# Kernel tuning notes

Hardware: AMD Instinct MI355X
Metric: run time of the kernel (lower is better)

## Reference

```python
import jax, jax.numpy as jnp
import numpy as np

IN_DIM = 300   # GloVe embedding dim
MEM = 150      # TreeLSTM memory dim
K = 4          # children per internal node (complete K-ary tree)
D = 9          # number of levels (leaves = level 0, root = level D-1)
SIZES = [K ** (D - 1 - d) for d in range(D)]  # nodes per level, leaves first
N = sum(SIZES)  # 87381 total nodes


def setup_inputs() -> dict:
    key = jax.random.key(0)
    ks = jax.random.split(key, 18)
    s_in = 1.0 / np.sqrt(IN_DIM)
    s_m = 1.0 / np.sqrt(MEM)
    inp = {"embs": jax.random.normal(ks[0], (N, IN_DIM), jnp.float32)}
    i = 1
    for nm in ["ix", "fx", "ux", "ox"]:  # input->mem linears
        inp["W_" + nm] = jax.random.uniform(ks[i], (IN_DIM, MEM), jnp.float32, -s_in, s_in); i += 1
        inp["b_" + nm] = jax.random.uniform(ks[i], (MEM,), jnp.float32, -s_in, s_in); i += 1
    for nm in ["ih", "fh", "uh", "oh"]:  # mem->mem linears
        inp["W_" + nm] = jax.random.uniform(ks[i], (MEM, MEM), jnp.float32, -s_m, s_m); i += 1
        inp["b_" + nm] = jax.random.uniform(ks[i], (MEM,), jnp.float32, -s_m, s_m); i += 1
    return inp


def reference(embs, W_ix, b_ix, W_fx, b_fx, W_ux, b_ux, W_ox, b_ox,
              W_ih, b_ih, W_fh, b_fh, W_uh, b_uh, W_oh, b_oh):
    """Level-batched Child-Sum TreeLSTM over a complete K-ary forest.
    Nodes are stored leaves-first; children of parent p at level d are
    nodes p*K .. p*K+K-1 of level d-1. Returns h for all N nodes (root last)."""
    off = 0
    h_prev = c_prev = None
    h_all = []
    for d in range(D):
        n = SIZES[d]
        x = embs[off:off + n]                       # (n, IN_DIM)
        if d == 0:
            # leaves: zero child state -> child_h_sum = 0, f*child_c = 0
            h_sum = jnp.zeros((n, MEM), embs.dtype)
            fc = jnp.zeros((n, MEM), embs.dtype)
        else:
            ch = h_prev.reshape(n, K, MEM)          # child h, (n, K, MEM)
            cc = c_prev.reshape(n, K, MEM)          # child c
            h_sum = ch.sum(axis=1)                  # child-sum of h
            # per-child forget gate: fh(child_h) + fx(x)
            f = jax.nn.sigmoid(jnp.einsum('nkm,mp->nkp', ch, W_fh) + b_fh
                               + (x @ W_fx + b_fx)[:, None, :])
            fc = (f * cc).sum(axis=1)
        i_g = jax.nn.sigmoid(x @ W_ix + b_ix + h_sum @ W_ih + b_ih)
        o_g = jax.nn.sigmoid(x @ W_ox + b_ox + h_sum @ W_oh + b_oh)
        u = jnp.tanh(x @ W_ux + b_ux + h_sum @ W_uh + b_uh)
        c = i_g * u + fc
        h = o_g * jnp.tanh(c)
        h_all.append(h)
        h_prev, c_prev = h, c
        off += n
    return jnp.concatenate(h_all, axis=0)           # (N, MEM)
```

## Files before the change

kernel.cpp:

```cpp
#include <hip/hip_runtime.h>

#define IN_DIM 300
#define MEM    150
#define GP     160
#define GW     640
#define KX     300
#define KXP    320
#define KH     160
#define NLEAF  65536
#define NTOT   87381
#define DEPTH  9

static const int SIZES[DEPTH] = {65536,16384,4096,1024,256,64,16,4,1};
static const int OFF[DEPTH]   = {0,65536,81920,86016,87040,87296,87360,87376,87380};

typedef __attribute__((ext_vector_type(8))) short short8;
typedef __attribute__((ext_vector_type(4))) float f32x4;

__device__ __forceinline__ float sigf(float x) { return 1.0f / (1.0f + __expf(-x)); }
__device__ __forceinline__ float tanhf_fast(float x) {
    float e = __expf(2.0f * x);
    return 1.0f - 2.0f / (e + 1.0f);
}
__device__ __forceinline__ unsigned short f2bf(float f) {
    union { float f; unsigned u; } v; v.f = f;
    unsigned r = v.u + 0x7FFF + ((v.u >> 16) & 1);
    return (unsigned short)(r >> 16);
}
__device__ __forceinline__ float bf2f(unsigned short u) {
    union { unsigned u; float f; } v; v.u = ((unsigned)u) << 16; return v.f;
}

typedef const __attribute__((address_space(1))) unsigned int* as1_u32p;
typedef __attribute__((address_space(3))) unsigned int* as3_u32p;
__device__ __forceinline__ void gl_lds16(const unsigned short* g, unsigned short* l) {
    __builtin_amdgcn_global_load_lds((as1_u32p)g, (as3_u32p)l, 16, 0, 0);
}

__global__ void pack_weights(const float* __restrict__ Wix, const float* __restrict__ Wfx,
                             const float* __restrict__ Wux, const float* __restrict__ Wox,
                             const float* __restrict__ bix, const float* __restrict__ bfx,
                             const float* __restrict__ bux, const float* __restrict__ box,
                             const float* __restrict__ Wih, const float* __restrict__ Wfh,
                             const float* __restrict__ Wuh, const float* __restrict__ Woh,
                             const float* __restrict__ bfh,
                             unsigned short* __restrict__ W4xT, unsigned short* __restrict__ W4hT,
                             float* __restrict__ b4x, float* __restrict__ b4hf)
{
    int stride = gridDim.x * blockDim.x;
    int tid = blockIdx.x * blockDim.x + threadIdx.x;
    for (int idx = tid; idx < GW * KXP; idx += stride) {
        int c = idx / KXP, k = idx - c * KXP;
        int g = c / GP, j = c - g * GP;
        const float* W = (g == 0) ? Wix : (g == 1) ? Wfx : (g == 2) ? Wux : Wox;
        W4xT[idx] = (j < MEM && k < KX) ? f2bf(W[k * MEM + j]) : (unsigned short)0;
    }
    for (int idx = tid; idx < GW * KH; idx += stride) {
        int c = idx / KH, k = idx - c * KH;
        int g = c / GP, j = c - g * GP;
        const float* W = (g == 0) ? Wih : (g == 1) ? Wfh : (g == 2) ? Wuh : Woh;
        W4hT[idx] = (j < MEM && k < MEM) ? f2bf(W[k * MEM + j]) : (unsigned short)0;
    }
    for (int idx = tid; idx < GW; idx += stride) {
        int g = idx / GP, j = idx - g * GP;
        const float* b = (g == 0) ? bix : (g == 1) ? bfx : (g == 2) ? bux : box;
        b4x[idx]  = (j < MEM) ? b[j] : 0.0f;
        b4hf[idx] = (g == 1 && j < MEM) ? bfh[j] : 0.0f;
    }
}

__global__ void conv_embs(const float* __restrict__ embs, unsigned short* __restrict__ Abf)
{
    int idx = blockIdx.x * 256 + threadIdx.x;
    if (idx >= NTOT * (KXP / 8)) return;
    int n = idx / (KXP / 8), c = idx - n * (KXP / 8);
    int c0 = c * 8;
    unsigned short v[8];
    if (c0 + 8 <= KX) {
        const float4* p = (const float4*)(embs + (size_t)n * KX + c0);
        float4 f0 = p[0], f1 = p[1];
        v[0]=f2bf(f0.x); v[1]=f2bf(f0.y); v[2]=f2bf(f0.z); v[3]=f2bf(f0.w);
        v[4]=f2bf(f1.x); v[5]=f2bf(f1.y); v[6]=f2bf(f1.z); v[7]=f2bf(f1.w);
    } else {
        const float* row = embs + (size_t)n * KX;
        #pragma unroll
        for (int j = 0; j < 8; ++j) {
            int col = c0 + j;
            v[j] = (col < KX) ? f2bf(row[col]) : (unsigned short)0;
        }
    }
    *(short8*)&Abf[(size_t)n * KXP + c0] = *(short8*)v;
}

template<int KPAD>
__global__ __launch_bounds__(256) void gemm_lds(
    const unsigned short* __restrict__ A, int M,
    const unsigned short* __restrict__ BT,
    const float* __restrict__ bias,
    unsigned short* __restrict__ Cout)
{
    __shared__ __align__(16) unsigned short As[2][128 * 32];
    __shared__ __align__(16) unsigned short Bs[2][128 * 32];

    const int nwg = gridDim.x;
    const int orig = blockIdx.x;
    const int qq = nwg >> 3, rr = nwg & 7;
    const int xcd = orig & 7, lin = orig >> 3;
    const int dd = (xcd < rr ? xcd * (qq + 1) : rr * (qq + 1) + (xcd - rr) * qq) + lin;
    const int mtile = dd / 5, ntile = dd - mtile * 5;

    const int t = threadIdx.x;
    const int m0 = mtile * 128, n0 = ntile * 128;
    const int l = t & 63, w = t >> 6;
    const int l15 = l & 15, q = l >> 4;
    const int wm = (w & 1) * 64, wn = (w >> 1) * 64;

    const int srow = t >> 2;
    const int scol = ((t & 3) ^ (srow & 3)) * 8;
    int gr0 = m0 + srow;      if (gr0 >= M) gr0 = M - 1;
    int gr1 = m0 + 64 + srow; if (gr1 >= M) gr1 = M - 1;
    const unsigned short* a0 = A + (size_t)gr0 * KPAD + scol;
    const unsigned short* a1 = A + (size_t)gr1 * KPAD + scol;
    const unsigned short* b0 = BT + (size_t)(n0 + srow) * KPAD + scol;
    const unsigned short* b1 = BT + (size_t)(n0 + 64 + srow) * KPAD + scol;

    f32x4 acc[4][4];
    #pragma unroll
    for (int i = 0; i < 4; ++i)
        #pragma unroll
        for (int j = 0; j < 4; ++j)
            acc[i][j] = (f32x4){0.f, 0.f, 0.f, 0.f};

    const int kiters = KPAD >> 5;
    gl_lds16(a0, &As[0][t * 8]);
    gl_lds16(a1, &As[0][2048 + t * 8]);
    gl_lds16(b0, &Bs[0][t * 8]);
    gl_lds16(b1, &Bs[0][2048 + t * 8]);
    __syncthreads();

    int cur = 0;
    for (int kt = 0; kt < kiters; ++kt) {
        if (kt + 1 < kiters) {
            const int ko = (kt + 1) << 5;
            const int nb = cur ^ 1;
            gl_lds16(a0 + ko, &As[nb][t * 8]);
            gl_lds16(a1 + ko, &As[nb][2048 + t * 8]);
            gl_lds16(b0 + ko, &Bs[nb][t * 8]);
            gl_lds16(b1 + ko, &Bs[nb][2048 + t * 8]);
        }
        short8 a[4], b[4];
        const int csw = (q ^ (l15 & 3)) * 8;
        #pragma unroll
        for (int i = 0; i < 4; ++i)
            a[i] = *(const short8*)&As[cur][(wm + i * 16 + l15) * 32 + csw];
        #pragma unroll
        for (int j = 0; j < 4; ++j)
            b[j] = *(const short8*)&Bs[cur][(wn + j * 16 + l15) * 32 + csw];
        #pragma unroll
        for (int i = 0; i < 4; ++i)
            #pragma unroll
            for (int j = 0; j < 4; ++j)
                acc[i][j] = __builtin_amdgcn_mfma_f32_16x16x32_bf16(a[i], b[j], acc[i][j], 0, 0, 0);
        __syncthreads();
        cur ^= 1;
    }

    float bj[4];
    #pragma unroll
    for (int j = 0; j < 4; ++j) bj[j] = bias[n0 + wn + j * 16 + l15];
    #pragma unroll
    for (int i = 0; i < 4; ++i) {
        #pragma unroll
        for (int r = 0; r < 4; ++r) {
            int grow = m0 + wm + i * 16 + q * 4 + r;
            if (grow < M) {
                unsigned short* crow = Cout + (size_t)grow * GW;
                #pragma unroll
                for (int j = 0; j < 4; ++j)
                    crow[n0 + wn + j * 16 + l15] = f2bf(acc[i][j][r] + bj[j]);
            }
        }
    }
}

__global__ void leaf_ew(const unsigned short* __restrict__ PG,
                        const float* __restrict__ bih, const float* __restrict__ buh,
                        const float* __restrict__ boh,
                        float* __restrict__ out, float* __restrict__ C,
                        unsigned short* __restrict__ Hbf)
{
    int idx = blockIdx.x * 256 + threadIdx.x;
    if (idx >= NLEAF * MEM) return;
    int n = idx / MEM, m = idx - n * MEM;
    const unsigned short* row = PG + (size_t)n * GW;
    float ip = bf2f(row[m])          + bih[m];
    float up = bf2f(row[2 * GP + m]) + buh[m];
    float op = bf2f(row[3 * GP + m]) + boh[m];
    float i = sigf(ip), u = tanhf_fast(up), o = sigf(op);
    float c = i * u;
    float h = o * tanhf_fast(c);
    out[idx] = h;
    C[idx] = c;
    Hbf[(size_t)n * KH + m] = f2bf(h);
    if (m < KH - MEM) Hbf[(size_t)n * KH + MEM + m] = 0;
}

__global__ void level_ew(const unsigned short* __restrict__ G,
                         const unsigned short* __restrict__ P,
                         const float* __restrict__ Cprev,
                         const float* __restrict__ bih, const float* __restrict__ buh,
                         const float* __restrict__ boh,
                         float* __restrict__ outRow, float* __restrict__ Crow,
                         unsigned short* __restrict__ HbfRow, int n)
{
    int idx = blockIdx.x * 256 + threadIdx.x;
    if (idx >= n * MEM) return;
    int nn = idx / MEM, m = idx - nn * MEM;
    const unsigned short* xr = P + (size_t)nn * GW;
    float ip = bf2f(xr[m]) + bih[m];
    float fx = bf2f(xr[GP + m]);
    float up = bf2f(xr[2 * GP + m]) + buh[m];
    float op = bf2f(xr[3 * GP + m]) + boh[m];
    float fc = 0.0f;
    #pragma unroll
    for (int k = 0; k < 4; ++k) {
        const unsigned short* gr = G + (size_t)(4 * nn + k) * GW;
        ip += bf2f(gr[m]);
        up += bf2f(gr[2 * GP + m]);
        op += bf2f(gr[3 * GP + m]);
        float f = sigf(fx + bf2f(gr[GP + m]));
        fc += f * Cprev[(4 * nn + k) * MEM + m];
    }
    float i = sigf(ip), u = tanhf_fast(up), o = sigf(op);
    float c = i * u + fc;
    float h = o * tanhf_fast(c);
    outRow[idx] = h;
    Crow[idx] = c;
    HbfRow[(size_t)nn * KH + m] = f2bf(h);
    if (m < KH - MEM) HbfRow[(size_t)nn * KH + MEM + m] = 0;
}

extern "C" void kernel_launch(void* const* d_in, const int* in_sizes, int n_in,
                              void* d_out, int out_size, void* d_ws, size_t ws_size,
                              hipStream_t stream)
{
    (void)in_sizes; (void)n_in; (void)out_size;
    const float* embs = (const float*)d_in[0];
    const float* Wix = (const float*)d_in[1];  const float* bix = (const float*)d_in[2];
    const float* Wfx = (const float*)d_in[3];  const float* bfx = (const float*)d_in[4];
    const float* Wux = (const float*)d_in[5];  const float* bux = (const float*)d_in[6];
    const float* Wox = (const float*)d_in[7];  const float* box = (const float*)d_in[8];
    const float* Wih = (const float*)d_in[9];  const float* bih = (const float*)d_in[10];
    const float* Wfh = (const float*)d_in[11]; const float* bfh = (const float*)d_in[12];
    const float* Wuh = (const float*)d_in[13]; const float* buh = (const float*)d_in[14];
    const float* Woh = (const float*)d_in[15]; const float* boh = (const float*)d_in[16];
    float* out = (float*)d_out;

    char* p = (char*)d_ws;
    auto alloc = [&](size_t bytes) -> char* {
        char* r = p;
        p += (bytes + 255) & ~(size_t)255;
        return r;
    };
    unsigned short* PG   = (unsigned short*)alloc((size_t)NTOT * GW * 2);
    float*          C    = (float*)alloc((size_t)NTOT * MEM * 4);
    unsigned short* Hbf  = (unsigned short*)alloc((size_t)NTOT * KH * 2);
    unsigned short* W4xT = (unsigned short*)alloc((size_t)GW * KXP * 2);
    unsigned short* W4hT = (unsigned short*)alloc((size_t)GW * KH * 2);
    float*          b4x  = (float*)alloc(GW * 4);
    float*          b4hf = (float*)alloc(GW * 4);
    if ((size_t)(p - (char*)d_ws) > ws_size) return;

    unsigned short* Abf = (unsigned short*)C;

    pack_weights<<<128, 256, 0, stream>>>(Wix, Wfx, Wux, Wox, bix, bfx, bux, box,
                                          Wih, Wfh, Wuh, Woh, bfh,
                                          W4xT, W4hT, b4x, b4hf);

    conv_embs<<<(NTOT * (KXP / 8) + 255) / 256, 256, 0, stream>>>(embs, Abf);

    {
        int mt = (NTOT + 127) / 128;
        gemm_lds<KXP><<<mt * 5, 256, 0, stream>>>(Abf, NTOT, W4xT, b4x, PG);
    }

    leaf_ew<<<(NLEAF * MEM + 255) / 256, 256, 0, stream>>>(PG, bih, buh, boh, out, C, Hbf);

    for (int d = 1; d < DEPTH; ++d) {
        int nprev = SIZES[d - 1];
        int n = SIZES[d];
        int mt = (nprev + 127) / 128;
        gemm_lds<KH><<<mt * 5, 256, 0, stream>>>(
            Hbf + (size_t)OFF[d - 1] * KH, nprev, W4hT, b4hf, PG);
        level_ew<<<(n * MEM + 255) / 256, 256, 0, stream>>>(
            PG, PG + (size_t)OFF[d] * GW,
            C + (size_t)OFF[d - 1] * MEM,
            bih, buh, boh,
            out + (size_t)OFF[d] * MEM, C + (size_t)OFF[d] * MEM,
            Hbf + (size_t)OFF[d] * KH, n);
    }
}
```

Baseline: 431.1 us.

## Deepen GEMM LDS pipeline to four stages with explicit vmcnt waits

Replaces the double-buffered direct-to-LDS load loop in the bf16 MFMA GEMM with a 4-buffer ring that keeps three K-slices of global loads in flight. It uses hand-placed s_waitcnt vmcnt thresholds and raw s_barrier instead of __syncthreads, and fully unrolls the K loop. It also raises wave priority around the MFMA block. The aim is to hide global-load latency better in the input-projection GEMM. In exchange LDS use doubles to 64KB, which may reduce occupancy, and correctness depends on exact vmcnt counting.

After: 440.7 us. 2.2% more time.

```diff
diff --git a/kernel.cpp b/kernel.cpp
--- a/kernel.cpp
+++ b/kernel.cpp
@@ -99,8 +99,8 @@
     const float* __restrict__ bias,
     unsigned short* __restrict__ Cout)
 {
-    __shared__ __align__(16) unsigned short As[2][128 * 32];
-    __shared__ __align__(16) unsigned short Bs[2][128 * 32];
+    __shared__ __align__(16) unsigned short As[4][4096];
+    __shared__ __align__(16) unsigned short Bs[4][4096];
 
     const int nwg = gridDim.x;
     const int orig = blockIdx.x;
@@ -131,38 +131,49 @@
         for (int j = 0; j < 4; ++j)
             acc[i][j] = (f32x4){0.f, 0.f, 0.f, 0.f};
 
-    const int kiters = KPAD >> 5;
-    gl_lds16(a0, &As[0][t * 8]);
-    gl_lds16(a1, &As[0][2048 + t * 8]);
-    gl_lds16(b0, &Bs[0][t * 8]);
-    gl_lds16(b1, &Bs[0][2048 + t * 8]);
-    __syncthreads();
-
-    int cur = 0;
-    for (int kt = 0; kt < kiters; ++kt) {
-        if (kt + 1 < kiters) {
-            const int ko = (kt + 1) << 5;
-            const int nb = cur ^ 1;
-            gl_lds16(a0 + ko, &As[nb][t * 8]);
-            gl_lds16(a1 + ko, &As[nb][2048 + t * 8]);
-            gl_lds16(b0 + ko, &Bs[nb][t * 8]);
-            gl_lds16(b1 + ko, &Bs[nb][2048 + t * 8]);
-        }
+    auto issue = [&](int s) {
+        const int ko = s << 5;
+        const int b = s & 3;
+        gl_lds16(a0 + ko, &As[b][t * 8]);
+        gl_lds16(a1 + ko, &As[b][2048 + t * 8]);
+        gl_lds16(b0 + ko, &Bs[b][t * 8]);
+        gl_lds16(b1 + ko, &Bs[b][2048 + t * 8]);
+    };
+
+    const int NST = KPAD >> 5;
+    issue(0); issue(1); issue(2);
+
+    #pragma unroll
+    for (int kt = 0; kt < NST; ++kt) {
+        if (kt + 3 < NST) issue(kt + 3);
+        __builtin_amdgcn_sched_barrier(0);
+        const int rem = NST - 1 - kt;
+        if (rem >= 3)      asm volatile("s_waitcnt vmcnt(12)" ::: "memory");
+        else if (rem == 2) asm volatile("s_waitcnt vmcnt(8)" ::: "memory");
+        else if (rem == 1) asm volatile("s_waitcnt vmcnt(4)" ::: "memory");
+        else               asm volatile("s_waitcnt vmcnt(0)" ::: "memory");
+        __builtin_amdgcn_s_barrier();
+        __builtin_amdgcn_sched_barrier(0);
+
+        const unsigned short* Ab = As[kt & 3];
+        const unsigned short* Bb = Bs[kt & 3];
         short8 a[4], b[4];
         const int csw = (q ^ (l15 & 3)) * 8;
         #pragma unroll
         for (int i = 0; i < 4; ++i)
-            a[i] = *(const short8*)&As[cur][(wm + i * 16 + l15) * 32 + csw];
+            a[i] = *(const short8*)&Ab[(wm + i * 16 + l15) * 32 + csw];
         #pragma unroll
         for (int j = 0; j < 4; ++j)
-            b[j] = *(const short8*)&Bs[cur][(wn + j * 16 + l15) * 32 + csw];
+            b[j] = *(const short8*)&Bb[(wn + j * 16 + l15) * 32 + csw];
+        __builtin_amdgcn_s_setprio(1);
         #pragma unroll
         for (int i = 0; i < 4; ++i)
             #pragma unroll
             for (int j = 0; j < 4; ++j)
                 acc[i][j] = __builtin_amdgcn_mfma_f32_16x16x32_bf16(a[i], b[j], acc[i][j], 0, 0, 0);
-        __syncthreads();
-        cur ^= 1;
+        __builtin_amdgcn_s_setprio(0);
+        __builtin_amdgcn_sched_barrier(0);
+        __builtin_amdgcn_s_barrier();
     }
 
     float bj[4];
```

## Fuse gate elementwise into GEMM epilogues via interleaved gate layout

Applied to the files above, without the earlier changes.

Reorders the packed weight columns so the four gates of each hidden unit sit next to each other. Each 128-column GEMM tile then holds every gate for 32 hidden units, so the leaf and level elementwise TreeLSTM math can run in the GEMM epilogue from LDS, removing the separate leaf_ew and level_ew kernels and the round trip of the per-child gate matrix through global memory. Leaf rows of the input projection are never written to PG, and the bf16 embedding buffer now reuses PG instead of C. The trade-off is a heavier epilogue with extra LDS staging and a barrier, and the aliasing of Abf onto PG must stay safe while tiles overwrite rows that other blocks may still be reading.

After: 371.8 us. 1.16x faster.

```diff
diff --git a/kernel.cpp b/kernel.cpp
--- a/kernel.cpp
+++ b/kernel.cpp
@@ -1,8 +1,6 @@
 #include <hip/hip_runtime.h>
 
-#define IN_DIM 300
 #define MEM    150
-#define GP     160
 #define GW     640
 #define KX     300
 #define KXP    320
@@ -51,18 +49,18 @@
     int tid = blockIdx.x * blockDim.x + threadIdx.x;
     for (int idx = tid; idx < GW * KXP; idx += stride) {
         int c = idx / KXP, k = idx - c * KXP;
-        int g = c / GP, j = c - g * GP;
+        int j = c >> 2, g = c & 3;
         const float* W = (g == 0) ? Wix : (g == 1) ? Wfx : (g == 2) ? Wux : Wox;
         W4xT[idx] = (j < MEM && k < KX) ? f2bf(W[k * MEM + j]) : (unsigned short)0;
     }
     for (int idx = tid; idx < GW * KH; idx += stride) {
         int c = idx / KH, k = idx - c * KH;
-        int g = c / GP, j = c - g * GP;
+        int j = c >> 2, g = c & 3;
         const float* W = (g == 0) ? Wih : (g == 1) ? Wfh : (g == 2) ? Wuh : Woh;
         W4hT[idx] = (j < MEM && k < MEM) ? f2bf(W[k * MEM + j]) : (unsigned short)0;
     }
     for (int idx = tid; idx < GW; idx += stride) {
-        int g = idx / GP, j = idx - g * GP;
+        int j = idx >> 2, g = idx & 3;
         const float* b = (g == 0) ? bix : (g == 1) ? bfx : (g == 2) ? bux : box;
         b4x[idx]  = (j < MEM) ? b[j] : 0.0f;
         b4hf[idx] = (g == 1 && j < MEM) ? bfh[j] : 0.0f;
@@ -92,15 +90,19 @@
     *(short8*)&Abf[(size_t)n * KXP + c0] = *(short8*)v;
 }
 
-template<int KPAD>
-__global__ __launch_bounds__(256) void gemm_lds(
-    const unsigned short* __restrict__ A, int M,
+__global__ __launch_bounds__(256) void gemm_xproj(
+    const unsigned short* __restrict__ A,
     const unsigned short* __restrict__ BT,
     const float* __restrict__ bias,
-    unsigned short* __restrict__ Cout)
+    unsigned short* __restrict__ PG,
+    const float* __restrict__ bih, const float* __restrict__ buh,
+    const float* __restrict__ boh,
+    float* __restrict__ outLeaf, float* __restrict__ CLeaf,
+    unsigned short* __restrict__ HbfLeaf)
 {
-    __shared__ __align__(16) unsigned short As[2][128 * 32];
-    __shared__ __align__(16) unsigned short Bs[2][128 * 32];
+    __shared__ __align__(16) unsigned short lds[16384];
+    unsigned short* As = lds;
+    unsigned short* Bs = lds + 8192;
 
     const int nwg = gridDim.x;
     const int orig = blockIdx.x;
@@ -117,12 +119,12 @@
 
     const int srow = t >> 2;
     const int scol = ((t & 3) ^ (srow & 3)) * 8;
-    int gr0 = m0 + srow;      if (gr0 >= M) gr0 = M - 1;
-    int gr1 = m0 + 64 + srow; if (gr1 >= M) gr1 = M - 1;
-    const unsigned short* a0 = A + (size_t)gr0 * KPAD + scol;
-    const unsigned short* a1 = A + (size_t)gr1 * KPAD + scol;
-    const unsigned short* b0 = BT + (size_t)(n0 + srow) * KPAD + scol;
-    const unsigned short* b1 = BT + (size_t)(n0 + 64 + srow) * KPAD + scol;
+    int gr0 = m0 + srow;      if (gr0 >= NTOT) gr0 = NTOT - 1;
+    int gr1 = m0 + 64 + srow; if (gr1 >= NTOT) gr1 = NTOT - 1;
+    const unsigned short* a0 = A + (size_t)gr0 * KXP + scol;
+    const unsigned short* a1 = A + (size_t)gr1 * KXP + scol;
+    const unsigned short* b0 = BT + (size_t)(n0 + srow) * KXP + scol;
+    const unsigned short* b1 = BT + (size_t)(n0 + 64 + srow) * KXP + scol;
 
     f32x4 acc[4][4];
     #pragma unroll
@@ -131,31 +133,31 @@
         for (int j = 0; j < 4; ++j)
             acc[i][j] = (f32x4){0.f, 0.f, 0.f, 0.f};
 
-    const int kiters = KPAD >> 5;
-    gl_lds16(a0, &As[0][t * 8]);
-    gl_lds16(a1, &As[0][2048 + t * 8]);
-    gl_lds16(b0, &Bs[0][t * 8]);
-    gl_lds16(b1, &Bs[0][2048 + t * 8]);
+    gl_lds16(a0, As + t * 8);
+    gl_lds16(a1, As + 2048 + t * 8);
+    gl_lds16(b0, Bs + t * 8);
+    gl_lds16(b1, Bs + 2048 + t * 8);
     __syncthreads();
 
     int cur = 0;
+    const int kiters = KXP >> 5;
     for (int kt = 0; kt < kiters; ++kt) {
         if (kt + 1 < kiters) {
             const int ko = (kt + 1) << 5;
             const int nb = cur ^ 1;
-            gl_lds16(a0 + ko, &As[nb][t * 8]);
-            gl_lds16(a1 + ko, &As[nb][2048 + t * 8]);
-            gl_lds16(b0 + ko, &Bs[nb][t * 8]);
-            gl_lds16(b1 + ko, &Bs[nb][2048 + t * 8]);
+            gl_lds16(a0 + ko, As + nb * 4096 + t * 8);
+            gl_lds16(a1 + ko, As + nb * 4096 + 2048 + t * 8);
+            gl_lds16(b0 + ko, Bs + nb * 4096 + t * 8);
+            gl_lds16(b1 + ko, Bs + nb * 4096 + 2048 + t * 8);
         }
         short8 a[4], b[4];
         const int csw = (q ^ (l15 & 3)) * 8;
         #pragma unroll
         for (int i = 0; i < 4; ++i)
-            a[i] = *(const short8*)&As[cur][(wm + i * 16 + l15) * 32 + csw];
-        #pragma unroll
-        for (int j = 0; j < 4; ++j)
-            b[j] = *(const short8*)&Bs[cur][(wn + j * 16 + l15) * 32 + csw];
+            a[i] = *(const short8*)&As[cur * 4096 + (wm + i * 16 + l15) * 32 + csw];
+        #pragma unroll
+        for (int j = 0; j < 4; ++j)
+            b[j] = *(const short8*)&Bs[cur * 4096 + (wn + j * 16 + l15) * 32 + csw];
         #pragma unroll
         for (int i = 0; i < 4; ++i)
             #pragma unroll
@@ -169,75 +171,174 @@
     #pragma unroll
     for (int j = 0; j < 4; ++j) bj[j] = bias[n0 + wn + j * 16 + l15];
     #pragma unroll
-    for (int i = 0; i < 4; ++i) {
-        #pragma unroll
-        for (int r = 0; r < 4; ++r) {
-            int grow = m0 + wm + i * 16 + q * 4 + r;
-            if (grow < M) {
-                unsigned short* crow = Cout + (size_t)grow * GW;
-                #pragma unroll
-                for (int j = 0; j < 4; ++j)
-                    crow[n0 + wn + j * 16 + l15] = f2bf(acc[i][j][r] + bj[j]);
+    for (int i = 0; i < 4; ++i)
+        #pragma unroll
+        for (int j = 0; j < 4; ++j)
+            #pragma unroll
+            for (int r = 0; r < 4; ++r)
+                lds[(wm + i * 16 + q * 4 + r) * 128 + wn + j * 16 + l15] =
+                    f2bf(acc[i][j][r] + bj[j]);
+    __syncthreads();
+
+    if (m0 < NLEAF) {
+        #pragma unroll
+        for (int s = 0; s < 16; ++s) {
+            int idx = (s << 8) + t;
+            int row = idx >> 5, jl = idx & 31;
+            int grow = m0 + row;
+            int j = ntile * 32 + jl;
+            const unsigned short* g4 = &lds[row * 128 + jl * 4];
+            if (j < MEM) {
+                float gi = bf2f(g4[0]) + bih[j];
+                float gu = bf2f(g4[2]) + buh[j];
+                float go = bf2f(g4[3]) + boh[j];
+                float iv = sigf(gi), uv = tanhf_fast(gu), ov = sigf(go);
+                float c = iv * uv;
+                float h = ov * tanhf_fast(c);
+                outLeaf[(size_t)grow * MEM + j] = h;
+                CLeaf[(size_t)grow * MEM + j] = c;
+                HbfLeaf[(size_t)grow * KH + j] = f2bf(h);
+            } else if (j < KH) {
+                HbfLeaf[(size_t)grow * KH + j] = 0;
             }
         }
-    }
-}
-
-__global__ void leaf_ew(const unsigned short* __restrict__ PG,
-                        const float* __restrict__ bih, const float* __restrict__ buh,
-                        const float* __restrict__ boh,
-                        float* __restrict__ out, float* __restrict__ C,
-                        unsigned short* __restrict__ Hbf)
+    } else {
+        int row = t >> 1, half = t & 1;
+        int grow = m0 + row;
+        if (grow < NTOT) {
+            const unsigned short* src = &lds[row * 128 + half * 64];
+            unsigned short* dst = PG + (size_t)grow * GW + n0 + half * 64;
+            #pragma unroll
+            for (int c8 = 0; c8 < 8; ++c8)
+                *(short8*)(dst + c8 * 8) = *(const short8*)(src + c8 * 8);
+        }
+    }
+}
+
+__global__ __launch_bounds__(256) void gemm_level(
+    const unsigned short* __restrict__ Hprev, int nprev, int npar,
+    const unsigned short* __restrict__ BT, const float* __restrict__ bias,
+    const unsigned short* __restrict__ P,
+    const float* __restrict__ Cprev,
+    const float* __restrict__ bih, const float* __restrict__ buh,
+    const float* __restrict__ boh,
+    float* __restrict__ outRow, float* __restrict__ Crow,
+    unsigned short* __restrict__ HbfRow)
 {
-    int idx = blockIdx.x * 256 + threadIdx.x;
-    if (idx >= NLEAF * MEM) return;
-    int n = idx / MEM, m = idx - n * MEM;
-    const unsigned short* row = PG + (size_t)n * GW;
-    float ip = bf2f(row[m])          + bih[m];
-    float up = bf2f(row[2 * GP + m]) + buh[m];
-    float op = bf2f(row[3 * GP + m]) + boh[m];
-    float i = sigf(ip), u = tanhf_fast(up), o = sigf(op);
-    float c = i * u;
-    float h = o * tanhf_fast(c);
-    out[idx] = h;
-    C[idx] = c;
-    Hbf[(size_t)n * KH + m] = f2bf(h);
-    if (m < KH - MEM) Hbf[(size_t)n * KH + MEM + m] = 0;
-}
-
-__global__ void level_ew(const unsigned short* __restrict__ G,
-                         const unsigned short* __restrict__ P,
-                         const float* __restrict__ Cprev,
-                         const float* __restrict__ bih, const float* __restrict__ buh,
-                         const float* __restrict__ boh,
-                         float* __restrict__ outRow, float* __restrict__ Crow,
-                         unsigned short* __restrict__ HbfRow, int n)
-{
-    int idx = blockIdx.x * 256 + threadIdx.x;
-    if (idx >= n * MEM) return;
-    int nn = idx / MEM, m = idx - nn * MEM;
-    const unsigned short* xr = P + (size_t)nn * GW;
-    float ip = bf2f(xr[m]) + bih[m];
-    float fx = bf2f(xr[GP + m]);
-    float up = bf2f(xr[2 * GP + m]) + buh[m];
-    float op = bf2f(xr[3 * GP + m]) + boh[m];
-    float fc = 0.0f;
-    #pragma unroll
-    for (int k = 0; k < 4; ++k) {
-        const unsigned short* gr = G + (size_t)(4 * nn + k) * GW;
-        ip += bf2f(gr[m]);
-        up += bf2f(gr[2 * GP + m]);
-        op += bf2f(gr[3 * GP + m]);
-        float f = sigf(fx + bf2f(gr[GP + m]));
-        fc += f * Cprev[(4 * nn + k) * MEM + m];
-    }
-    float i = sigf(ip), u = tanhf_fast(up), o = sigf(op);
-    float c = i * u + fc;
-    float h = o * tanhf_fast(c);
-    outRow[idx] = h;
-    Crow[idx] = c;
-    HbfRow[(size_t)nn * KH + m] = f2bf(h);
-    if (m < KH - MEM) HbfRow[(size_t)nn * KH + MEM + m] = 0;
+    __shared__ __align__(16) unsigned short lds[16384];
+    unsigned short* As = lds;
+    unsigned short* Bs = lds + 8192;
+
+    const int nwg = gridDim.x;
+    const int orig = blockIdx.x;
+    const int qq = nwg >> 3, rr = nwg & 7;
+    const int xcd = orig & 7, lin = orig >> 3;
+    const int dd = (xcd < rr ? xcd * (qq + 1) : rr * (qq + 1) + (xcd - rr) * qq) + lin;
+    const int mtile = dd / 5, ntile = dd - mtile * 5;
+
+    const int t = threadIdx.x;
+    const int m0 = mtile * 128, n0 = ntile * 128;
+    const int l = t & 63, w = t >> 6;
+    const int l15 = l & 15, q = l >> 4;
+    const int wm = (w & 1) * 64, wn = (w >> 1) * 64;
+
+    const int srow = t >> 2;
+    const int scol = ((t & 3) ^ (srow & 3)) * 8;
+    int gr0 = m0 + srow;      if (gr0 >= nprev) gr0 = nprev - 1;
+    int gr1 = m0 + 64 + srow; if (gr1 >= nprev) gr1 = nprev - 1;
+    const unsigned short* a0 = Hprev + (size_t)gr0 * KH + scol;
+    const unsigned short* a1 = Hprev + (size_t)gr1 * KH + scol;
+    const unsigned short* b0 = BT + (size_t)(n0 + srow) * KH + scol;
+    const unsigned short* b1 = BT + (size_t)(n0 + 64 + srow) * KH + scol;
+
+    f32x4 acc[4][4];
+    #pragma unroll
+    for (int i = 0; i < 4; ++i)
+        #pragma unroll
+        for (int j = 0; j < 4; ++j)
+            acc[i][j] = (f32x4){0.f, 0.f, 0.f, 0.f};
+
+    gl_lds16(a0, As + t * 8);
+    gl_lds16(a1, As + 2048 + t * 8);
+    gl_lds16(b0, Bs + t * 8);
+    gl_lds16(b1, Bs + 2048 + t * 8);
+    __syncthreads();
+
+    int cur = 0;
+    const int kiters = KH >> 5;
+    for (int kt = 0; kt < kiters; ++kt) {
+        if (kt + 1 < kiters) {
+            const int ko = (kt + 1) << 5;
+            const int nb = cur ^ 1;
+            gl_lds16(a0 + ko, As + nb * 4096 + t * 8);
+            gl_lds16(a1 + ko, As + nb * 4096 + 2048 + t * 8);
+            gl_lds16(b0 + ko, Bs + nb * 4096 + t * 8);
+            gl_lds16(b1 + ko, Bs + nb * 4096 + 2048 + t * 8);
+        }
+        short8 a[4], b[4];
+        const int csw = (q ^ (l15 & 3)) * 8;
+        #pragma unroll
+        for (int i = 0; i < 4; ++i)
+            a[i] = *(const short8*)&As[cur * 4096 + (wm + i * 16 + l15) * 32 + csw];
+        #pragma unroll
+        for (int j = 0; j < 4; ++j)
+            b[j] = *(const short8*)&Bs[cur * 4096 + (wn + j * 16 + l15) * 32 + csw];
+        #pragma unroll
+        for (int i = 0; i < 4; ++i)
+            #pragma unroll
+            for (int j = 0; j < 4; ++j)
+                acc[i][j] = __builtin_amdgcn_mfma_f32_16x16x32_bf16(a[i], b[j], acc[i][j], 0, 0, 0);
+        __syncthreads();
+        cur ^= 1;
+    }
+
+    float bj[4];
+    #pragma unroll
+    for (int j = 0; j < 4; ++j) bj[j] = bias[n0 + wn + j * 16 + l15];
+    #pragma unroll
+    for (int i = 0; i < 4; ++i)
+        #pragma unroll
+        for (int j = 0; j < 4; ++j)
+            #pragma unroll
+            for (int r = 0; r < 4; ++r)
+                lds[(wm + i * 16 + q * 4 + r) * 128 + wn + j * 16 + l15] =
+                    f2bf(acc[i][j][r] + bj[j]);
+    __syncthreads();
+
+    const int pp0 = m0 >> 2;
+    #pragma unroll
+    for (int s = 0; s < 4; ++s) {
+        int idx = (s << 8) + t;
+        int pl = idx >> 5, jl = idx & 31;
+        int par = pp0 + pl;
+        if (par >= npar) continue;
+        int j = ntile * 32 + jl;
+        if (j < MEM) {
+            const unsigned short* xr = P + (size_t)par * GW + 4 * j;
+            float ip = bf2f(xr[0]) + bih[j];
+            float fx = bf2f(xr[1]);
+            float up = bf2f(xr[2]) + buh[j];
+            float op = bf2f(xr[3]) + boh[j];
+            float fc = 0.0f;
+            #pragma unroll
+            for (int k = 0; k < 4; ++k) {
+                const unsigned short* g4 = &lds[(pl * 4 + k) * 128 + jl * 4];
+                ip += bf2f(g4[0]);
+                up += bf2f(g4[2]);
+                op += bf2f(g4[3]);
+                float f = sigf(fx + bf2f(g4[1]));
+                fc += f * Cprev[(size_t)(4 * par + k) * MEM + j];
+            }
+            float iv = sigf(ip), uv = tanhf_fast(up), ov = sigf(op);
+            float c = iv * uv + fc;
+            float h = ov * tanhf_fast(c);
+            outRow[(size_t)par * MEM + j] = h;
+            Crow[(size_t)par * MEM + j] = c;
+            HbfRow[(size_t)par * KH + j] = f2bf(h);
+        } else if (j < KH) {
+            HbfRow[(size_t)par * KH + j] = 0;
+        }
+    }
 }
 
 extern "C" void kernel_launch(void* const* d_in, const int* in_sizes, int n_in,
@@ -271,7 +372,7 @@
     float*          b4hf = (float*)alloc(GW * 4);
     if ((size_t)(p - (char*)d_ws) > ws_size) return;
 
-    unsigned short* Abf = (unsigned short*)C;
+    unsigned short* Abf = PG;
 
     pack_weights<<<128, 256, 0, stream>>>(Wix, Wfx, Wux, Wox, bix, bfx, bux, box,
                                           Wih, Wfh, Wuh, Woh, bfh,
@@ -281,22 +382,21 @@
 
     {
         int mt = (NTOT + 127) / 128;
-        gemm_lds<KXP><<<mt * 5, 256, 0, stream>>>(Abf, NTOT, W4xT, b4x, PG);
-    }
-
-    leaf_ew<<<(NLEAF * MEM + 255) / 256, 256, 0, stream>>>(PG, bih, buh, boh, out, C, Hbf);
+        gemm_xproj<<<mt * 5, 256, 0, stream>>>(
+            Abf, W4xT, b4x, PG, bih, buh, boh, out, C, Hbf);
+    }
 
     for (int d = 1; d < DEPTH; ++d) {
         int nprev = SIZES[d - 1];
         int n = SIZES[d];
         int mt = (nprev + 127) / 128;
-        gemm_lds<KH><<<mt * 5, 256, 0, stream>>>(
-            Hbf + (size_t)OFF[d - 1] * KH, nprev, W4hT, b4hf, PG);
-        level_ew<<<(n * MEM + 255) / 256, 256, 0, stream>>>(
-            PG, PG + (size_t)OFF[d] * GW,
+        gemm_level<<<mt * 5, 256, 0, stream>>>(
+            Hbf + (size_t)OFF[d - 1] * KH, nprev, n,
+            W4hT, b4hf,
+            PG + (size_t)OFF[d] * GW,
             C + (size_t)OFF[d - 1] * MEM,
             bih, buh, boh,
             out + (size_t)OFF[d] * MEM, C + (size_t)OFF[d] * MEM,
-            Hbf + (size_t)OFF[d] * KH, n);
-    }
-}
+            Hbf + (size_t)OFF[d] * KH);
+    }
+}
```
